# Performance work log

Measured on AMD Instinct MI355X. Metric: run time of the kernel, lower is better.

Reference implementation:

```python
import jax, jax.numpy as jnp
import numpy as np

B, N, C, T = 512, 62, 8, 64
K = 8          # topk
HEADS = 4
OUT = 128
EPS = 1e-5     # BatchNorm1d eps
NEG_SLOPE = 0.2  # GATConv leaky_relu slope


def _gat(x, W, a_src, a_dst, bias, src, dst, valid, num_nodes, concat):
    """PyG GATConv (eval mode, self-loops already in edge list)."""
    H, Co = a_src.shape[1], a_src.shape[2]
    xl = (x @ W.T).reshape(num_nodes, H, Co)          # [V,H,Co]
    al_src = jnp.sum(xl * a_src, axis=-1)             # [V,H]
    al_dst = jnp.sum(xl * a_dst, axis=-1)             # [V,H]
    alpha = jax.nn.leaky_relu(al_src[src] + al_dst[dst], NEG_SLOPE)  # [E,H]
    alpha = jnp.where(valid[:, None], alpha, -jnp.inf)
    amax = jax.ops.segment_max(alpha, dst, num_segments=num_nodes)   # [V,H]
    ex = jnp.where(valid[:, None], jnp.exp(alpha - amax[dst]), 0.0)
    denom = jax.ops.segment_sum(ex, dst, num_segments=num_nodes)     # [V,H]
    w = ex / denom[dst]                                              # softmax per dst
    out = jax.ops.segment_sum(xl[src] * w[:, :, None], dst, num_segments=num_nodes)
    out = out.reshape(num_nodes, H * Co) if concat else out.mean(axis=1)
    return out + bias


def reference(x, edge_index, W1, W2, b_sp, V_sp, bn_w, bn_b,
              g1_w, g1_asrc, g1_adst, g1_b, g2_w, g2_asrc, g2_adst, g2_b):
    # edge_index is unused: spatial=True rebuilds the graph from attention.
    x4 = x.reshape(B, N, C, T)
    # SpatialAttention: ((x @ W1) @ W2) -> tanh(. @ V + b) -> BatchNorm1d(N)
    prod = jnp.einsum('bnct,t->bnc', x4, W1) @ W2      # [B,N,N]
    S = jnp.tanh(prod @ V_sp + b_sp)                   # [B,N,N]
    mean = S.mean(axis=(0, 2), keepdims=True)          # BN over channel dim 1
    var = S.var(axis=(0, 2), keepdims=True)
    adj = (S - mean) / jnp.sqrt(var + EPS) * bn_w[None, :, None] + bn_b[None, :, None]
    # topk mask + dense_to_sparse: exactly K edges per (batch, row)
    _, idx = jax.lax.top_k(adj, K)                     # [B,N,K] column indices
    offs = (jnp.arange(B) * N)[:, None, None]
    src = (jnp.broadcast_to(jnp.arange(N)[None, :, None], (B, N, K)) + offs).reshape(-1)
    dst = (idx + offs).reshape(-1)
    # GATConv: remove_self_loops then add_self_loops -> mask topk self-edges, append loops
    loops = jnp.arange(B * N)
    valid = jnp.concatenate([src != dst, jnp.ones(B * N, dtype=bool)])
    src = jnp.concatenate([src, loops])
    dst = jnp.concatenate([dst, loops])
    h = x4.reshape(B * N, C * T)
    h = jax.nn.relu(_gat(h, g1_w, g1_asrc, g1_adst, g1_b, src, dst, valid, B * N, True))
    h = jax.nn.relu(_gat(h, g2_w, g2_asrc, g2_adst, g2_b, src, dst, valid, B * N, False))
    return h


def setup_inputs() -> dict:
    key = jax.random.key(0)
    ks = jax.random.split(key, 16)
    d_in = C * T  # 512
    return {
        'x': jax.random.normal(ks[0], (B, N, C, T), jnp.float32),
        'edge_index': jax.random.randint(ks[1], (2, 128), 0, B * N, jnp.int64) if False else jax.random.randint(ks[1], (2, 128), 0, B * N).astype(jnp.int32),
        'W1': jax.random.uniform(ks[2], (T,), jnp.float32),
        'W2': jax.random.normal(ks[3], (C, N), jnp.float32) * 0.1,
        'b_sp': jax.random.normal(ks[4], (1, N, N), jnp.float32) * 0.1,
        'V_sp': jax.random.normal(ks[5], (N, N), jnp.float32) * 0.1,
        'bn_w': jnp.ones((N,), jnp.float32),
        'bn_b': jnp.zeros((N,), jnp.float32),
        'g1_w': jax.random.normal(ks[6], (HEADS * OUT, d_in), jnp.float32) * 0.04,
        'g1_asrc': jax.random.normal(ks[7], (1, HEADS, OUT), jnp.float32) * 0.06,
        'g1_adst': jax.random.normal(ks[8], (1, HEADS, OUT), jnp.float32) * 0.06,
        'g1_b': jnp.zeros((HEADS * OUT,), jnp.float32),
        'g2_w': jax.random.normal(ks[9], (HEADS * OUT, HEADS * OUT), jnp.float32) * 0.04,
        'g2_asrc': jax.random.normal(ks[10], (1, HEADS, OUT), jnp.float32) * 0.06,
        'g2_adst': jax.random.normal(ks[11], (1, HEADS, OUT), jnp.float32) * 0.06,
        'g2_b': jnp.zeros((OUT,), jnp.float32),
    }
```

## Files before the change

kernel.cpp:

```cpp
#include <hip/hip_runtime.h>
#include <math.h>

#define B_ 512
#define N_ 62
#define V_ (B_ * N_)
#define TOPK_ 8

typedef __attribute__((ext_vector_type(8))) short bf16x8;
typedef __attribute__((ext_vector_type(4))) float f32x4;

__device__ __forceinline__ unsigned short bf16rn(float f) {
    unsigned int u = __float_as_uint(f);
    unsigned int r = (u + 0x7fffu + ((u >> 16) & 1u)) >> 16;
    return (unsigned short)r;
}
__device__ __forceinline__ float bf16tof(unsigned short h) {
    return __uint_as_float(((unsigned int)h) << 16);
}

__device__ __forceinline__ void gload16(const void* g, void* l) {
    __builtin_amdgcn_global_load_lds(
        (const __attribute__((address_space(1))) unsigned int*)g,
        (__attribute__((address_space(3))) unsigned int*)l, 16, 0, 0);
}

__global__ __launch_bounds__(64) void spatial_S(
    const float* __restrict__ x, const float* __restrict__ W1,
    const float* __restrict__ W2, const float* __restrict__ bsp,
    const float* __restrict__ Vsp, float* __restrict__ S)
{
    int blk = blockIdx.x;
    int n = blk % N_;
    int lane = threadIdx.x;
    const float* xr = x + (size_t)blk * 512;
    float w1 = W1[lane];

    float y[8];
#pragma unroll
    for (int c = 0; c < 8; ++c) {
        float p = xr[c * 64 + lane] * w1;
#pragma unroll
        for (int off = 32; off; off >>= 1) p += __shfl_xor(p, off);
        y[c] = p;
    }

    __shared__ float pr[N_];
    if (lane < N_) {
        float acc = 0.f;
#pragma unroll
        for (int c = 0; c < 8; ++c) acc += y[c] * W2[c * N_ + lane];
        pr[lane] = acc;
    }
    __syncthreads();
    if (lane < N_) {
        float acc = bsp[n * N_ + lane];
        for (int k = 0; k < N_; ++k) acc += pr[k] * Vsp[k * N_ + lane];
        S[(size_t)blk * N_ + lane] = tanhf(acc);
    }
}

__global__ __launch_bounds__(256) void bn_part(
    const float* __restrict__ S, double* __restrict__ part)
{
    int n = blockIdx.x >> 4, slice = blockIdx.x & 15;
    double s = 0.0, s2 = 0.0;
    int i0 = slice * 1984;
    for (int i = i0 + threadIdx.x; i < i0 + 1984; i += 256) {
        int b = i / N_, m = i - b * N_;
        float v = S[((size_t)b * N_ + n) * N_ + m];
        s += v; s2 += (double)v * v;
    }
    __shared__ double sh[256], sh2[256];
    sh[threadIdx.x] = s; sh2[threadIdx.x] = s2;
    __syncthreads();
    for (int off = 128; off; off >>= 1) {
        if (threadIdx.x < off) {
            sh[threadIdx.x] += sh[threadIdx.x + off];
            sh2[threadIdx.x] += sh2[threadIdx.x + off];
        }
        __syncthreads();
    }
    if (threadIdx.x == 0) {
        part[((size_t)n * 16 + slice) * 2 + 0] = sh[0];
        part[((size_t)n * 16 + slice) * 2 + 1] = sh2[0];
    }
}

__global__ __launch_bounds__(64) void bn_final(
    const double* __restrict__ part, const float* __restrict__ bnw,
    const float* __restrict__ bnb, float* __restrict__ scale,
    float* __restrict__ shift)
{
    int n = threadIdx.x;
    if (n >= N_) return;
    double s = 0.0, s2 = 0.0;
    for (int j = 0; j < 16; ++j) {
        s  += part[((size_t)n * 16 + j) * 2 + 0];
        s2 += part[((size_t)n * 16 + j) * 2 + 1];
    }
    const double cnt = (double)(B_ * N_);
    double mean = s / cnt;
    double var = s2 / cnt - mean * mean;
    float inv = (float)(1.0 / sqrt(var + 1e-5));
    scale[n] = bnw[n] * inv;
    shift[n] = bnb[n] - (float)mean * bnw[n] * inv;
}

__global__ __launch_bounds__(64) void topk_mask(
    const float* __restrict__ S, const float* __restrict__ scale,
    const float* __restrict__ shift, unsigned long long* __restrict__ maskT)
{
    int blk = blockIdx.x;
    int b = blk / N_, n = blk - b * N_;
    int lane = threadIdx.x;
    float v = (lane < N_) ? S[(size_t)blk * N_ + lane] * scale[n] + shift[n]
                          : -INFINITY;
    bool sel = false;
#pragma unroll
    for (int k = 0; k < TOPK_; ++k) {
        float mv = v; int mi = lane;
#pragma unroll
        for (int off = 32; off; off >>= 1) {
            float ov = __shfl_xor(mv, off);
            int   oi = __shfl_xor(mi, off);
            if (ov > mv || (ov == mv && oi < mi)) { mv = ov; mi = oi; }
        }
        if (lane == mi) { sel = true; v = -INFINITY; }
    }
    unsigned long long row = __ballot(sel) | (1ull << n);
    if (lane < N_ && ((row >> lane) & 1ull))
        atomicOr(&maskT[(size_t)b * N_ + lane], 1ull << n);
}

__global__ __launch_bounds__(256) void zero_u64(unsigned long long* p, int n)
{
    int i = blockIdx.x * 256 + threadIdx.x;
    if (i < n) p[i] = 0ull;
}

__global__ __launch_bounds__(256) void split_hi(
    const float* __restrict__ in, unsigned short* __restrict__ out, int total4)
{
    int gid = blockIdx.x * 256 + threadIdx.x;
    if (gid >= total4) return;
    float4 v = ((const float4*)in)[gid];
    ushort4 h;
    h.x = bf16rn(v.x); h.y = bf16rn(v.y); h.z = bf16rn(v.z); h.w = bf16rn(v.w);
    ((ushort4*)out)[gid] = h;
}

__global__ __launch_bounds__(256) void split_pair(
    const float* __restrict__ in, unsigned short* __restrict__ out, int total4)
{
    int gid = blockIdx.x * 256 + threadIdx.x;
    if (gid >= total4) return;
    int row = gid >> 7;
    int c = (gid & 127) * 4;
    float4 v = ((const float4*)in)[gid];
    ushort4 h, l;
    float f;
    h.x = bf16rn(v.x); f = v.x - bf16tof(h.x); l.x = bf16rn(f);
    h.y = bf16rn(v.y); f = v.y - bf16tof(h.y); l.y = bf16rn(f);
    h.z = bf16rn(v.z); f = v.z - bf16tof(h.z); l.z = bf16rn(f);
    h.w = bf16rn(v.w); f = v.w - bf16tof(h.w); l.w = bf16rn(f);
    *(ushort4*)(&out[(size_t)row * 1024 + c])       = h;
    *(ushort4*)(&out[(size_t)row * 1024 + 512 + c]) = l;
}

__global__ __launch_bounds__(256) void gemm_bf16(
    const unsigned short* __restrict__ Ah, const unsigned short* __restrict__ Bw,
    unsigned short* __restrict__ Cs)
{
    __shared__ __align__(16) unsigned short smem[16384];
    char* As = (char*)smem;
    char* Bs = (char*)(smem + 8192);

    int tid = threadIdx.x;
    int lane = tid & 63, w = tid >> 6;

    int flat = blockIdx.y * 4 + blockIdx.x;
    int swz = (flat & 7) * 124 + (flat >> 3);
    int by = swz >> 2, bx = swz & 3;
    int bm = by * 128, bn = bx * 128;

    int wr = w >> 1, wc = w & 1;

    f32x4 acc[4][4];
#pragma unroll
    for (int mf = 0; mf < 4; ++mf)
#pragma unroll
        for (int nf = 0; nf < 4; ++nf) acc[mf][nf] = (f32x4){0.f, 0.f, 0.f, 0.f};

    int srow = w * 8 + (lane >> 3);
    int kcol = (lane & 7) ^ (lane >> 3);
    int ldsoff = w * 1024;

    for (int kt = 0; kt < 16; ++kt) {
        int k0 = (kt & 7) * 64;
        int bBase = (kt >> 3) * 512 + k0;
#pragma unroll
        for (int i = 0; i < 4; ++i) {
            int row = i * 32 + srow;
            gload16(Ah + (size_t)(bm + row) * 512 + k0 + kcol * 8,
                    As + i * 4096 + ldsoff);
            gload16(Bw + (size_t)(bn + row) * 1024 + bBase + kcol * 8,
                    Bs + i * 4096 + ldsoff);
        }
        __syncthreads();

#pragma unroll
        for (int kk = 0; kk < 2; ++kk) {
            bf16x8 af[4], bfr[4];
#pragma unroll
            for (int mf = 0; mf < 4; ++mf)
                af[mf] = *(const bf16x8*)(As + (wr*64 + mf*16 + (lane&15))*128
                                             + ((kk*4 + (lane>>4)) ^ (lane&7))*16);
#pragma unroll
            for (int nf = 0; nf < 4; ++nf)
                bfr[nf] = *(const bf16x8*)(Bs + (wc*64 + nf*16 + (lane&15))*128
                                              + ((kk*4 + (lane>>4)) ^ (lane&7))*16);
#pragma unroll
            for (int mf = 0; mf < 4; ++mf)
#pragma unroll
                for (int nf = 0; nf < 4; ++nf)
                    acc[mf][nf] = __builtin_amdgcn_mfma_f32_16x16x32_bf16(
                        af[mf], bfr[nf], acc[mf][nf], 0, 0, 0);
        }
        __syncthreads();
    }

    int r0 = bm + wr * 64 + (lane >> 4) * 4;
    int c0 = bn + wc * 64 + (lane & 15);
#pragma unroll
    for (int mf = 0; mf < 4; ++mf)
#pragma unroll
        for (int nf = 0; nf < 4; ++nf)
#pragma unroll
            for (int r = 0; r < 4; ++r) {
                float v = acc[mf][nf][r];
                unsigned short h = bf16rn(v);
                unsigned short l = bf16rn(v - bf16tof(h));
                size_t row = (size_t)(r0 + mf * 16 + r);
                Cs[row * 1024 + c0 + nf * 16] = h;
                Cs[row * 1024 + 512 + c0 + nf * 16] = l;
            }
}

template <int LAYER>
__global__ __launch_bounds__(512, 4) void gat_agg2(
    const unsigned short* __restrict__ XL,
    const float* __restrict__ asrc, const float* __restrict__ adst,
    const unsigned long long* __restrict__ maskT,
    const float* __restrict__ bias, void* __restrict__ outp)
{
    __shared__ __align__(16) float smem[16368];
    float* wls = smem;
    float* shs = smem + 15872;
    float* shd = smem + 15872 + 248;

    int b = blockIdx.x;
    int tid = threadIdx.x;
    int lane = tid & 63, w = tid >> 6;
    const unsigned short* base = XL + (size_t)b * N_ * 1024;

    for (int t = w; t < 248; t += 8) {
        int s = t >> 2, h = t & 3;
        const unsigned short* xv = base + (size_t)s * 1024 + h * 128;
        float x0 = bf16tof(xv[lane])      + bf16tof(xv[512 + lane]);
        float x1 = bf16tof(xv[64 + lane]) + bf16tof(xv[576 + lane]);
        float ps = x0 * asrc[h * 128 + lane] + x1 * asrc[h * 128 + 64 + lane];
        float pd = x0 * adst[h * 128 + lane] + x1 * adst[h * 128 + 64 + lane];
#pragma unroll
        for (int off = 32; off; off >>= 1) {
            ps += __shfl_xor(ps, off);
            pd += __shfl_xor(pd, off);
        }
        if (lane == 0) { shs[t] = ps; shd[t] = pd; }
    }
    __syncthreads();

    for (int t = w; t < 248; t += 8) {
        int d = t >> 2, h = t & 3;
        unsigned long long m = maskT[(size_t)b * N_ + d];
        bool valid = (lane < N_) && ((m >> lane) & 1ull);
        float a = -INFINITY;
        if (valid) {
            float raw = shs[lane * 4 + h] + shd[d * 4 + h];
            a = (raw > 0.f) ? raw : 0.2f * raw;
        }
        float mx = a;
#pragma unroll
        for (int off = 32; off; off >>= 1) mx = fmaxf(mx, __shfl_xor(mx, off));
        float ex = valid ? expf(a - mx) : 0.f;
        float sm = ex;
#pragma unroll
        for (int off = 32; off; off >>= 1) sm += __shfl_xor(sm, off);
        if (lane < N_) wls[((size_t)h * N_ + lane) * 64 + d] = ex / sm;
    }
    __syncthreads();

    int hc = tid >> 7;
    float acc[62];
#pragma unroll
    for (int d = 0; d < 62; ++d) acc[d] = 0.f;

    for (int s = 0; s < N_; ++s) {
        float x = bf16tof(base[(size_t)s * 1024 + tid])
                + bf16tof(base[(size_t)s * 1024 + 512 + tid]);
        const float* wp = &wls[((size_t)hc * N_ + s) * 64];
#pragma unroll
        for (int g = 0; g < 15; ++g) {
            float4 w4 = *(const float4*)(wp + g * 4);
            acc[4*g+0] += w4.x * x;
            acc[4*g+1] += w4.y * x;
            acc[4*g+2] += w4.z * x;
            acc[4*g+3] += w4.w * x;
        }
        float2 w2 = *(const float2*)(wp + 60);
        acc[60] += w2.x * x;
        acc[61] += w2.y * x;
    }

    if (LAYER == 1) {
        float bct = bias[tid];
        unsigned short* H = (unsigned short*)outp + (size_t)b * N_ * 512;
#pragma unroll
        for (int d = 0; d < 62; ++d) {
            float v = acc[d] + bct;
            v = v > 0.f ? v : 0.f;
            H[(size_t)d * 512 + tid] = bf16rn(v);
        }
    } else {
        __syncthreads();
        float* red = smem;
        float* outf = (float*)outp;
#pragma unroll
        for (int d0 = 0; d0 < 64; d0 += 16) {
#pragma unroll
            for (int di = 0; di < 16; ++di) {
                int d = d0 + di;
                if (d < 62) red[di * 512 + tid] = acc[d];
            }
            __syncthreads();
            int cnt = (62 - d0) < 16 ? (62 - d0) : 16;
            for (int i = tid; i < cnt * 128; i += 512) {
                int di = i >> 7, c = i & 127;
                float s4 = (red[di*512 + c] + red[di*512 + 128 + c] +
                            red[di*512 + 256 + c] + red[di*512 + 384 + c]) * 0.25f
                           + bias[c];
                outf[((size_t)b * N_ + d0 + di) * 128 + c] = s4 > 0.f ? s4 : 0.f;
            }
            __syncthreads();
        }
    }
}

extern "C" void kernel_launch(void* const* d_in, const int* in_sizes, int n_in,
                              void* d_out, int out_size, void* d_ws, size_t ws_size,
                              hipStream_t stream)
{
    const float* x    = (const float*)d_in[0];
    const float* W1   = (const float*)d_in[2];
    const float* W2   = (const float*)d_in[3];
    const float* bsp  = (const float*)d_in[4];
    const float* Vsp  = (const float*)d_in[5];
    const float* bnw  = (const float*)d_in[6];
    const float* bnb  = (const float*)d_in[7];
    const float* g1w  = (const float*)d_in[8];
    const float* g1as = (const float*)d_in[9];
    const float* g1ad = (const float*)d_in[10];
    const float* g1b  = (const float*)d_in[11];
    const float* g2w  = (const float*)d_in[12];
    const float* g2as = (const float*)d_in[13];
    const float* g2ad = (const float*)d_in[14];
    const float* g2b  = (const float*)d_in[15];
    float* out = (float*)d_out;

    char* ws = (char*)d_ws;
    size_t off = 0;
    auto alloc = [&](size_t bytes) -> void* {
        void* p = ws + off;
        off += (bytes + 255) & ~(size_t)255;
        return p;
    };
    float* S      = (float*)alloc((size_t)V_ * N_ * 4);
    float* scale  = (float*)alloc(N_ * 4);
    float* shift  = (float*)alloc(N_ * 4);
    double* part  = (double*)alloc((size_t)N_ * 16 * 2 * 8);
    unsigned long long* maskT = (unsigned long long*)alloc((size_t)V_ * 8);
    unsigned short* A2  = (unsigned short*)alloc((size_t)V_ * 512 * 2);
    unsigned short* Bw1 = (unsigned short*)alloc((size_t)512 * 1024 * 2);
    unsigned short* Bw2 = (unsigned short*)alloc((size_t)512 * 1024 * 2);
    unsigned short* XL  = (unsigned short*)alloc((size_t)V_ * 1024 * 2);
    unsigned short* H1  = (unsigned short*)alloc((size_t)V_ * 512 * 2);

    zero_u64<<<(V_ + 255) / 256, 256, 0, stream>>>(maskT, V_);
    spatial_S<<<V_, 64, 0, stream>>>(x, W1, W2, bsp, Vsp, S);
    bn_part<<<N_ * 16, 256, 0, stream>>>(S, part);
    bn_final<<<1, 64, 0, stream>>>(part, bnw, bnb, scale, shift);
    topk_mask<<<V_, 64, 0, stream>>>(S, scale, shift, maskT);

    split_hi<<<(V_ * 128 + 255) / 256, 256, 0, stream>>>(x, A2, V_ * 128);
    split_pair<<<(512 * 128 + 255) / 256, 256, 0, stream>>>(g1w, Bw1, 512 * 128);
    split_pair<<<(512 * 128 + 255) / 256, 256, 0, stream>>>(g2w, Bw2, 512 * 128);

    dim3 gg(4, 248);
    gemm_bf16<<<gg, 256, 0, stream>>>(A2, Bw1, XL);
    gat_agg2<1><<<B_, 512, 0, stream>>>(XL, g1as, g1ad, maskT, g1b, H1);

    gemm_bf16<<<gg, 256, 0, stream>>>(H1, Bw2, XL);
    gat_agg2<2><<<B_, 512, 0, stream>>>(XL, g2as, g2ad, maskT, g2b, out);
}
```

Baseline: 481.5 us.

## Use MFMA for GAT aggregation and fuse x bf16 conversion into spatial kernel

The per-block GAT aggregation loop, previously 62 scalar FMA accumulators per thread, becomes bf16 MFMA matrix multiplies. Attention weights are stored as bf16 in a swizzled LDS layout, and the hi/lo split of XL is kept via two MFMAs. The layer-2 head-mean and ReLU move into a separate small kernel working on an intermediate bf16 buffer, and the separate x-to-bf16 conversion kernel is folded into spatial_S. This trades precision, since attention weights and the layer-2 output are now rounded to bf16, and adds an extra intermediate buffer pass.

After: 407.6 us. 15.4% less time.

```diff
diff --git a/kernel.cpp b/kernel.cpp
--- a/kernel.cpp
+++ b/kernel.cpp
@@ -27,7 +27,8 @@
 __global__ __launch_bounds__(64) void spatial_S(
     const float* __restrict__ x, const float* __restrict__ W1,
     const float* __restrict__ W2, const float* __restrict__ bsp,
-    const float* __restrict__ Vsp, float* __restrict__ S)
+    const float* __restrict__ Vsp, float* __restrict__ S,
+    unsigned short* __restrict__ A2)
 {
     int blk = blockIdx.x;
     int n = blk % N_;
@@ -38,7 +39,9 @@
     float y[8];
 #pragma unroll
     for (int c = 0; c < 8; ++c) {
-        float p = xr[c * 64 + lane] * w1;
+        float xv = xr[c * 64 + lane];
+        A2[(size_t)blk * 512 + c * 64 + lane] = bf16rn(xv);
+        float p = xv * w1;
 #pragma unroll
         for (int off = 32; off; off >>= 1) p += __shfl_xor(p, off);
         y[c] = p;
@@ -136,17 +139,6 @@
 {
     int i = blockIdx.x * 256 + threadIdx.x;
     if (i < n) p[i] = 0ull;
-}
-
-__global__ __launch_bounds__(256) void split_hi(
-    const float* __restrict__ in, unsigned short* __restrict__ out, int total4)
-{
-    int gid = blockIdx.x * 256 + threadIdx.x;
-    if (gid >= total4) return;
-    float4 v = ((const float4*)in)[gid];
-    ushort4 h;
-    h.x = bf16rn(v.x); h.y = bf16rn(v.y); h.z = bf16rn(v.z); h.w = bf16rn(v.w);
-    ((ushort4*)out)[gid] = h;
 }
 
 __global__ __launch_bounds__(256) void split_pair(
@@ -246,17 +238,17 @@
             }
 }
 
-template <int LAYER>
-__global__ __launch_bounds__(512, 4) void gat_agg2(
+template <int APPLY>
+__global__ __launch_bounds__(512, 4) void gat_aggM(
     const unsigned short* __restrict__ XL,
     const float* __restrict__ asrc, const float* __restrict__ adst,
     const unsigned long long* __restrict__ maskT,
-    const float* __restrict__ bias, void* __restrict__ outp)
-{
-    __shared__ __align__(16) float smem[16368];
-    float* wls = smem;
-    float* shs = smem + 15872;
-    float* shd = smem + 15872 + 248;
+    const float* __restrict__ bias,
+    unsigned short* __restrict__ H)
+{
+    __shared__ __align__(16) char lds[34816];
+    float* shs = (float*)(lds + 32768);
+    float* shd = (float*)(lds + 33760);
 
     int b = blockIdx.x;
     int tid = threadIdx.x;
@@ -295,64 +287,77 @@
         float sm = ex;
 #pragma unroll
         for (int off = 32; off; off >>= 1) sm += __shfl_xor(sm, off);
-        if (lane < N_) wls[((size_t)h * N_ + lane) * 64 + d] = ex / sm;
+        float wv = valid ? ex / sm : 0.f;
+        int addr = h * 8192 + d * 128
+                 + (((lane >> 3) ^ (d & 7)) << 4) + ((lane & 7) << 1);
+        *(unsigned short*)(lds + addr) = bf16rn(wv);
     }
     __syncthreads();
 
-    int hc = tid >> 7;
-    float acc[62];
-#pragma unroll
-    for (int d = 0; d < 62; ++d) acc[d] = 0.f;
-
-    for (int s = 0; s < N_; ++s) {
-        float x = bf16tof(base[(size_t)s * 1024 + tid])
-                + bf16tof(base[(size_t)s * 1024 + 512 + tid]);
-        const float* wp = &wls[((size_t)hc * N_ + s) * 64];
-#pragma unroll
-        for (int g = 0; g < 15; ++g) {
-            float4 w4 = *(const float4*)(wp + g * 4);
-            acc[4*g+0] += w4.x * x;
-            acc[4*g+1] += w4.y * x;
-            acc[4*g+2] += w4.z * x;
-            acc[4*g+3] += w4.w * x;
-        }
-        float2 w2 = *(const float2*)(wp + 60);
-        acc[60] += w2.x * x;
-        acc[61] += w2.y * x;
-    }
-
-    if (LAYER == 1) {
-        float bct = bias[tid];
-        unsigned short* H = (unsigned short*)outp + (size_t)b * N_ * 512;
-#pragma unroll
-        for (int d = 0; d < 62; ++d) {
-            float v = acc[d] + bct;
-            v = v > 0.f ? v : 0.f;
-            H[(size_t)d * 512 + tid] = bf16rn(v);
-        }
-    } else {
-        __syncthreads();
-        float* red = smem;
-        float* outf = (float*)outp;
-#pragma unroll
-        for (int d0 = 0; d0 < 64; d0 += 16) {
-#pragma unroll
-            for (int di = 0; di < 16; ++di) {
-                int d = d0 + di;
-                if (d < 62) red[di * 512 + tid] = acc[d];
+    int cc = lane & 15, lh = lane >> 4;
+
+    union U8 { unsigned short s[8]; bf16x8 v; };
+
+#pragma unroll
+    for (int ch = 0; ch < 4; ++ch) {
+        f32x4 acc[4];
+#pragma unroll
+        for (int mf = 0; mf < 4; ++mf) acc[mf] = (f32x4){0.f, 0.f, 0.f, 0.f};
+
+        const unsigned short* xp = base + (size_t)(lh * 8) * 1024
+                                        + ch * 128 + w * 16 + cc;
+#pragma unroll
+        for (int kk = 0; kk < 2; ++kk) {
+            U8 bh, bl;
+#pragma unroll
+            for (int j = 0; j < 8; ++j) {
+                size_t o = (size_t)(kk * 32 + j) * 1024;
+                bh.s[j] = xp[o];
+                bl.s[j] = xp[o + 512];
             }
-            __syncthreads();
-            int cnt = (62 - d0) < 16 ? (62 - d0) : 16;
-            for (int i = tid; i < cnt * 128; i += 512) {
-                int di = i >> 7, c = i & 127;
-                float s4 = (red[di*512 + c] + red[di*512 + 128 + c] +
-                            red[di*512 + 256 + c] + red[di*512 + 384 + c]) * 0.25f
-                           + bias[c];
-                outf[((size_t)b * N_ + d0 + di) * 128 + c] = s4 > 0.f ? s4 : 0.f;
+            bf16x8 af[4];
+#pragma unroll
+            for (int mf = 0; mf < 4; ++mf)
+                af[mf] = *(const bf16x8*)(lds + ch * 8192
+                              + (mf * 16 + cc) * 128
+                              + (((kk * 4 + lh) ^ (cc & 7)) << 4));
+#pragma unroll
+            for (int mf = 0; mf < 4; ++mf) {
+                acc[mf] = __builtin_amdgcn_mfma_f32_16x16x32_bf16(
+                    af[mf], bh.v, acc[mf], 0, 0, 0);
+                acc[mf] = __builtin_amdgcn_mfma_f32_16x16x32_bf16(
+                    af[mf], bl.v, acc[mf], 0, 0, 0);
             }
-            __syncthreads();
-        }
-    }
+        }
+
+        int c = ch * 128 + w * 16 + cc;
+        float bc = APPLY ? bias[c] : 0.f;
+#pragma unroll
+        for (int mf = 0; mf < 4; ++mf)
+#pragma unroll
+            for (int r = 0; r < 4; ++r) {
+                int d = mf * 16 + lh * 4 + r;
+                if (d < N_) {
+                    float v = acc[mf][r] + bc;
+                    if (APPLY) v = v > 0.f ? v : 0.f;
+                    H[(size_t)(b * N_ + d) * 512 + c] = bf16rn(v);
+                }
+            }
+    }
+}
+
+__global__ __launch_bounds__(512) void mean_relu(
+    const unsigned short* __restrict__ H2, const float* __restrict__ bias,
+    float* __restrict__ out)
+{
+    int tid = threadIdx.x;
+    int v = blockIdx.x * 4 + (tid >> 7);
+    int c = tid & 127;
+    const unsigned short* t = H2 + (size_t)v * 512;
+    float s = bf16tof(t[c]) + bf16tof(t[128 + c]) +
+              bf16tof(t[256 + c]) + bf16tof(t[384 + c]);
+    s = s * 0.25f + bias[c];
+    out[(size_t)v * 128 + c] = s > 0.f ? s : 0.f;
 }
 
 extern "C" void kernel_launch(void* const* d_in, const int* in_sizes, int n_in,
@@ -391,23 +396,24 @@
     unsigned short* A2  = (unsigned short*)alloc((size_t)V_ * 512 * 2);
     unsigned short* Bw1 = (unsigned short*)alloc((size_t)512 * 1024 * 2);
     unsigned short* Bw2 = (unsigned short*)alloc((size_t)512 * 1024 * 2);
-    unsigned short* XL  = (unsigned short*)alloc((size_t)V_ * 1024 * 2);
+    unsigned short* XL  = (unsigned short*)alloc((size_t)(V_ + 2) * 1024 * 2);
     unsigned short* H1  = (unsigned short*)alloc((size_t)V_ * 512 * 2);
+    unsigned short* H2  = (unsigned short*)alloc((size_t)V_ * 512 * 2);
 
     zero_u64<<<(V_ + 255) / 256, 256, 0, stream>>>(maskT, V_);
-    spatial_S<<<V_, 64, 0, stream>>>(x, W1, W2, bsp, Vsp, S);
+    spatial_S<<<V_, 64, 0, stream>>>(x, W1, W2, bsp, Vsp, S, A2);
     bn_part<<<N_ * 16, 256, 0, stream>>>(S, part);
     bn_final<<<1, 64, 0, stream>>>(part, bnw, bnb, scale, shift);
     topk_mask<<<V_, 64, 0, stream>>>(S, scale, shift, maskT);
 
-    split_hi<<<(V_ * 128 + 255) / 256, 256, 0, stream>>>(x, A2, V_ * 128);
     split_pair<<<(512 * 128 + 255) / 256, 256, 0, stream>>>(g1w, Bw1, 512 * 128);
     split_pair<<<(512 * 128 + 255) / 256, 256, 0, stream>>>(g2w, Bw2, 512 * 128);
 
     dim3 gg(4, 248);
     gemm_bf16<<<gg, 256, 0, stream>>>(A2, Bw1, XL);
-    gat_agg2<1><<<B_, 512, 0, stream>>>(XL, g1as, g1ad, maskT, g1b, H1);
+    gat_aggM<1><<<B_, 512, 0, stream>>>(XL, g1as, g1ad, maskT, g1b, H1);
 
     gemm_bf16<<<gg, 256, 0, stream>>>(H1, Bw2, XL);
-    gat_agg2<2><<<B_, 512, 0, stream>>>(XL, g2as, g2ad, maskT, g2b, out);
-}
+    gat_aggM<0><<<B_, 512, 0, stream>>>(XL, g2as, g2ad, maskT, g2b, H2);
+    mean_relu<<<V_ / 4, 512, 0, stream>>>(H2, g2b, out);
+}
```
